# Kernel optimization log

Measured on AMD Instinct MI355X. Metric: run time of the kernel, lower is better.

## Reference

```python
import jax, jax.numpy as jnp
import numpy as np

IN, H, L = 512, 1024, 2
N, T = 64, 256


def setup_inputs() -> dict:
    key = jax.random.key(0)
    ks = jax.random.split(key, 1 + 4 * L)
    x = jax.random.normal(ks[0], (N, T, IN), dtype=jnp.float32)
    inp = {"x": x}
    for l in range(L):
        d_in = IN if l == 0 else H
        s_x = 1.0 / np.sqrt(d_in)
        s_h = 1.0 / np.sqrt(H)
        # concatenated gate order: [i, f, g, o]
        inp[f"Wx{l}"] = jax.random.normal(ks[1 + 4 * l], (4 * H, d_in), dtype=jnp.float32) * s_x
        inp[f"Wh{l}"] = jax.random.normal(ks[2 + 4 * l], (4 * H, H), dtype=jnp.float32) * s_h
        inp[f"b{l}"] = jax.random.normal(ks[3 + 4 * l], (4 * H,), dtype=jnp.float32) * 0.1
        # peephole weights for [i, f, o] (original inits these to zero; randomized here)
        inp[f"Wc{l}"] = jax.random.normal(ks[4 + 4 * l], (3, H), dtype=jnp.float32) * 0.1
    return inp


def _lstm_forward(x, params):
    # params: list of (Wx [4H,d_in], Wh [4H,H], b [4H], Wc [3,H]) per layer
    n = x.shape[0]
    h0 = jnp.zeros((L, n, H), dtype=x.dtype)
    c0 = jnp.zeros((L, n, H), dtype=x.dtype)

    def step(carry, x_t):
        hs, cs = carry
        new_h, new_c = [], []
        inp_t = x_t
        for l, (Wx, Wh, b, Wc) in enumerate(params):
            h, c = hs[l], cs[l]
            gates = inp_t @ Wx.T + h @ Wh.T + b  # [n, 4H]
            gi, gf, gg, go = jnp.split(gates, 4, axis=-1)
            i = jax.nn.sigmoid(gi + Wc[0] * c)
            f = jax.nn.sigmoid(gf + Wc[1] * c)  # computed but unused (faithful to source)
            g = jnp.tanh(gg)
            o = jax.nn.sigmoid(go + Wc[2] * c)
            ct = g * c + i * g          # faithful: forget gate not applied
            ht = o * jnp.tanh(c)        # faithful: uses OLD cell state
            new_h.append(ht)
            new_c.append(ct)
            inp_t = ht  # dropout p=0 -> identity
        hs = jnp.stack(new_h)
        cs = jnp.stack(new_c)
        return (hs, cs), new_h[-1]

    (hs, cs), outs = jax.lax.scan(step, (h0, c0), jnp.swapaxes(x, 0, 1))
    out = jnp.swapaxes(outs, 0, 1)  # [N, T, H]
    return out, (hs[-1], cs[-1])


def reference(x, Wx0, Wh0, b0, Wc0, Wx1, Wh1, b1, Wc1):
    params = [(Wx0, Wh0, b0, Wc0), (Wx1, Wh1, b1, Wc1)]
    return _lstm_forward(x, params)
```

## Files before the change

kernel.cpp:

```cpp
#include <hip/hip_runtime.h>
#include <stdint.h>


#define T_STEPS 256
#define HDIM    1024
#define NB      64
#define INDIM   512
#define NWG     256
#define TPB     256
#define PRING   8

typedef _Float16 f16;
typedef __attribute__((ext_vector_type(8))) _Float16 f16x8;
typedef __attribute__((ext_vector_type(4))) float    f32x4;

#define CNT_OFF 0
#define XB_OFF  81920
#define H0_OFF  16859136
#define H1_OFF  50544640
#define C0_OFF  84230144
#define C1_OFF  84492288
#define P0_OFF  84754432
#define P1_OFF  91045888

__device__ __forceinline__ float sigm(float x)     { return 1.0f / (1.0f + __expf(-x)); }
__device__ __forceinline__ float tanhfast(float x) { float e = __expf(2.0f * x); return 1.0f - 2.0f / (e + 1.0f); }

__device__ __forceinline__ void arrive(int* c) {
  __hip_atomic_fetch_add(c, 1, __ATOMIC_RELAXED, __HIP_MEMORY_SCOPE_AGENT);
}
__device__ __forceinline__ void wait_ge(int* c, int v) {
  while (__hip_atomic_load(c, __ATOMIC_RELAXED, __HIP_MEMORY_SCOPE_AGENT) < v)
    __builtin_amdgcn_s_sleep(1);
  __atomic_signal_fence(__ATOMIC_ACQUIRE);
}
__device__ __forceinline__ void sti(int* p, int v) {
  __hip_atomic_store(p, v, __ATOMIC_RELAXED, __HIP_MEMORY_SCOPE_AGENT);
}
__device__ __forceinline__ void st2h(f16* p, float a, float b) {
  union { f16 h[2]; uint32_t u; } cc; cc.h[0] = (f16)a; cc.h[1] = (f16)b;
  __hip_atomic_store((uint32_t*)p, cc.u, __ATOMIC_RELAXED, __HIP_MEMORY_SCOPE_AGENT);
}
__device__ __forceinline__ void st8a(void* p, unsigned long long v) {
  __hip_atomic_store((unsigned long long*)p, v, __ATOMIC_RELAXED, __HIP_MEMORY_SCOPE_AGENT);
}
__device__ __forceinline__ unsigned long long ld8(const float* p) {
  return __hip_atomic_load((const unsigned long long*)p, __ATOMIC_RELAXED, __HIP_MEMORY_SCOPE_AGENT);
}
__device__ __forceinline__ f16x8 pack8(f32x4 a, f32x4 b) {
  f16x8 h;
  h[0]=(f16)a[0]; h[1]=(f16)a[1]; h[2]=(f16)a[2]; h[3]=(f16)a[3];
  h[4]=(f16)b[0]; h[5]=(f16)b[1]; h[6]=(f16)b[2]; h[7]=(f16)b[3];
  return h;
}

template<int K>
__device__ __forceinline__ void gemm48_regB(const f16* __restrict__ Aw,
                                            const f16x8 (&B)[3][8],
                                            int lr, f32x4 (&acc)[4][3]) {
  constexpr int NIT = K / 128;
  const f16* a0 = Aw + (size_t)(lr +  0) * K;
  const f16* a1 = Aw + (size_t)(lr + 16) * K;
  const f16* a2 = Aw + (size_t)(lr + 32) * K;
  const f16* a3 = Aw + (size_t)(lr + 48) * K;
  f16x8 A0[NIT], A1[NIT], A2[NIT], A3[NIT];
#pragma unroll
  for (int it = 0; it < NIT; ++it) {
    const int kk = it * 32;
    A0[it] = *(const f16x8*)(a0 + kk);
    A1[it] = *(const f16x8*)(a1 + kk);
    A2[it] = *(const f16x8*)(a2 + kk);
    A3[it] = *(const f16x8*)(a3 + kk);
  }
#pragma unroll
  for (int it = 0; it < NIT; ++it) {
    acc[0][0] = __builtin_amdgcn_mfma_f32_16x16x32_f16(A0[it], B[0][it], acc[0][0], 0, 0, 0);
    acc[0][1] = __builtin_amdgcn_mfma_f32_16x16x32_f16(A0[it], B[1][it], acc[0][1], 0, 0, 0);
    acc[0][2] = __builtin_amdgcn_mfma_f32_16x16x32_f16(A0[it], B[2][it], acc[0][2], 0, 0, 0);
    acc[1][0] = __builtin_amdgcn_mfma_f32_16x16x32_f16(A1[it], B[0][it], acc[1][0], 0, 0, 0);
    acc[1][1] = __builtin_amdgcn_mfma_f32_16x16x32_f16(A1[it], B[1][it], acc[1][1], 0, 0, 0);
    acc[1][2] = __builtin_amdgcn_mfma_f32_16x16x32_f16(A1[it], B[2][it], acc[1][2], 0, 0, 0);
    acc[2][0] = __builtin_amdgcn_mfma_f32_16x16x32_f16(A2[it], B[0][it], acc[2][0], 0, 0, 0);
    acc[2][1] = __builtin_amdgcn_mfma_f32_16x16x32_f16(A2[it], B[1][it], acc[2][1], 0, 0, 0);
    acc[2][2] = __builtin_amdgcn_mfma_f32_16x16x32_f16(A2[it], B[2][it], acc[2][2], 0, 0, 0);
    acc[3][0] = __builtin_amdgcn_mfma_f32_16x16x32_f16(A3[it], B[0][it], acc[3][0], 0, 0, 0);
    acc[3][1] = __builtin_amdgcn_mfma_f32_16x16x32_f16(A3[it], B[1][it], acc[3][1], 0, 0, 0);
    acc[3][2] = __builtin_amdgcn_mfma_f32_16x16x32_f16(A3[it], B[2][it], acc[3][2], 0, 0, 0);
  }
}

__global__ __launch_bounds__(TPB, 1) void lstm_pers(
    const float* __restrict__ x,
    const float* __restrict__ Wx0, const float* __restrict__ Wh0,
    const float* __restrict__ b0,  const float* __restrict__ Wc0,
    const float* __restrict__ Wx1, const float* __restrict__ Wh1,
    const float* __restrict__ b1,  const float* __restrict__ Wc1,
    float* __restrict__ out, char* __restrict__ ws)
{
  int* cbase = (int*)(ws + CNT_OFF);
  int* proCnt = cbase;
  auto FLG = [&](int g, int i) { return cbase + 16 + ((g * 64 + i) << 4); };

  f16* XB   = (f16*)(ws + XB_OFF);
  f16* H0   = (f16*)(ws + H0_OFF);
  f16* H1   = (f16*)(ws + H1_OFF);
  float* C0 = (float*)(ws + C0_OFF);
  float* C1 = (float*)(ws + C1_OFF);
  float* P0b = (float*)(ws + P0_OFF);
  float* P1b = (float*)(ws + P1_OFF);

  __shared__ float lds[4][64][52];

  const int tid  = threadIdx.x;
  const int wg   = blockIdx.x;
  const int gtid = wg * TPB + tid;
  const int GSZ  = NWG * TPB;

  const int grp  = wg >> 6;
  const int ug   = wg & 63;
  const int lane = tid & 63;
  const int wv   = tid >> 6;
  const int quad = lane >> 4;
  const int lr   = lane & 15;

  const float* Wsrc; int K;
  switch (grp) {
    case 0:  Wsrc = Wx0; K = 512;  break;
    case 1:  Wsrc = Wh0; K = 1024; break;
    case 2:  Wsrc = Wx1; K = 1024; break;
    default: Wsrc = Wh1; K = 1024; break;
  }
  const int Kq  = K >> 2;
  const int NIT = K >> 7;

  f16x8 Breg[3][8];
#pragma unroll
  for (int nt = 0; nt < 3; ++nt) {
    const int R = ug * 16 + lr + (nt == 1 ? 2048 : (nt == 2 ? 3072 : 0));
    const float* wr = Wsrc + (size_t)R * K + wv * Kq + quad * 8;
#pragma unroll
    for (int it = 0; it < 8; ++it) {
      if (it < NIT) {
        f32x4 f0 = *(const f32x4*)(wr + it * 32);
        f32x4 f1 = *(const f32x4*)(wr + it * 32 + 4);
        Breg[nt][it] = pack8(f0, f1);
      } else {
        Breg[nt][it] = (f16x8){};
      }
    }
  }
  for (int idx = gtid; idx < T_STEPS * NB * 256; idx += GSZ) {
    int t = idx >> 14, n = (idx >> 8) & 63, i2 = (idx & 255) << 1;
    const float* src = x + (size_t)n * (T_STEPS * INDIM) + (size_t)t * INDIM + i2;
    st2h(&XB[(size_t)idx << 1], src[0], src[1]);
  }

  __builtin_amdgcn_s_waitcnt(0);
  __syncthreads();
  if (tid == 0) { arrive(proCnt); wait_ge(proCnt, NWG); }
  __syncthreads();

  float* cst = (grp == 1) ? C0 : C1;
  const int m_e = tid >> 2, j0 = (tid & 3) << 2;
  const int u0  = ug * 16 + j0;
  float* crow = cst + (size_t)m_e * HDIM + u0;

  f32x4 b_i{}, b_g{}, b_o{}, wci{}, wco{};
  if (grp & 1) {
    const float* bb = (grp == 1) ? b0 : b1;
    const float* wc = (grp == 1) ? Wc0 : Wc1;
    b_i = *(const f32x4*)(bb + u0);
    b_g = *(const f32x4*)(bb + 2048 + u0);
    b_o = *(const f32x4*)(bb + 3072 + u0);
    wci = *(const f32x4*)(wc + u0);
    wco = *(const f32x4*)(wc + 2048 + u0);
  }

  for (int t = 0; t < T_STEPS; ++t) {
    {
      int* myp = nullptr; int tgt = 0;
      if (grp == 0) {
        if (lane == 0 && t >= PRING) { myp = FLG(1, ug); tgt = t - PRING + 1; }
      } else if (grp == 1) {
        if (lane < 16 && t > 0)      { myp = FLG(1, wv * 16 + lr); tgt = t; }
        else if (lane == 16)         { myp = FLG(0, ug); tgt = t + 1; }
      } else if (grp == 2) {
        if (lane < 16)               { myp = FLG(1, wv * 16 + lr); tgt = t + 1; }
        else if (lane == 16 && t >= PRING) { myp = FLG(3, ug); tgt = t - PRING + 1; }
      } else {
        if (lane < 16 && t > 0)      { myp = FLG(3, wv * 16 + lr); tgt = t; }
        else if (lane == 16)         { myp = FLG(2, ug); tgt = t + 1; }
      }
      if (myp) {
        while (__hip_atomic_load(myp, __ATOMIC_RELAXED, __HIP_MEMORY_SCOPE_AGENT) < tgt)
          __builtin_amdgcn_s_sleep(1);
      }
      __atomic_signal_fence(__ATOMIC_ACQUIRE);
    }

    const f16* Abase;
    if (grp == 0)      Abase = XB + (size_t)t * NB * INDIM;
    else if (grp == 1) Abase = H0 + (size_t)t * NB * HDIM;
    else if (grp == 2) Abase = H0 + (size_t)(t + 1) * NB * HDIM;
    else               Abase = H1 + (size_t)t * NB * HDIM;

    unsigned long long pr0, pr1, pr2, pr3, pr4, pr5;
    f32x4 c4{};
    if (grp & 1) {
      const float* Pb = (grp == 1 ? P0b : P1b) + (size_t)(t & (PRING - 1)) * NB * 3072;
      const float* pbase = Pb + (size_t)m_e * 3072 + ug * 48 + j0;
      pr0 = ld8(pbase);      pr1 = ld8(pbase + 2);
      pr2 = ld8(pbase + 16); pr3 = ld8(pbase + 18);
      pr4 = ld8(pbase + 32); pr5 = ld8(pbase + 34);
      c4 = *(const f32x4*)crow;
    }

    f32x4 acc[4][3];
#pragma unroll
    for (int mt = 0; mt < 4; ++mt)
#pragma unroll
      for (int nt = 0; nt < 3; ++nt)
        acc[mt][nt] = (f32x4){0.f, 0.f, 0.f, 0.f};

    const f16* Aw = Abase + wv * Kq + quad * 8;
    if (grp == 0) gemm48_regB<512>(Aw, Breg, lr, acc);
    else          gemm48_regB<1024>(Aw, Breg, lr, acc);

#pragma unroll
    for (int mt = 0; mt < 4; ++mt)
#pragma unroll
      for (int nt = 0; nt < 3; ++nt)
#pragma unroll
        for (int r = 0; r < 4; ++r)
          lds[wv][mt * 16 + quad * 4 + r][nt * 16 + lr] = acc[mt][nt][r];
    __syncthreads();

    f32x4 hv, cn;
    if ((grp & 1) == 0) {
      float* Pb = (grp == 0 ? P0b : P1b) + (size_t)(t & (PRING - 1)) * NB * 3072;
#pragma unroll
      for (int r = 0; r < 6; ++r) {
        const int s  = r * 256 + tid;
        const int m  = s / 24, cp = s - m * 24;
        const int c0 = cp << 1;
        float v0 = lds[0][m][c0]     + lds[1][m][c0]     + lds[2][m][c0]     + lds[3][m][c0];
        float v1 = lds[0][m][c0 + 1] + lds[1][m][c0 + 1] + lds[2][m][c0 + 1] + lds[3][m][c0 + 1];
        union { float f[2]; unsigned long long u; } pp; pp.f[0] = v0; pp.f[1] = v1;
        st8a(Pb + (size_t)m * 3072 + ug * 48 + c0, pp.u);
      }
    } else {
      union { unsigned long long u; float f[2]; } q0, q1, q2, q3, q4, q5;
      q0.u = pr0; q1.u = pr1; q2.u = pr2; q3.u = pr3; q4.u = pr4; q5.u = pr5;
      f32x4 vi = (f32x4){0.f, 0.f, 0.f, 0.f};
      f32x4 vg = vi, vo = vi;
#pragma unroll
      for (int w = 0; w < 4; ++w) {
        vi += *(const f32x4*)&lds[w][m_e][j0];
        vg += *(const f32x4*)&lds[w][m_e][16 + j0];
        vo += *(const f32x4*)&lds[w][m_e][32 + j0];
      }
      const float pif[4] = {q0.f[0], q0.f[1], q1.f[0], q1.f[1]};
      const float pgf[4] = {q2.f[0], q2.f[1], q3.f[0], q3.f[1]};
      const float pof[4] = {q4.f[0], q4.f[1], q5.f[0], q5.f[1]};
      f16* Hdst = (grp == 1 ? H0 : H1) + (size_t)(t + 1) * NB * HDIM;
#pragma unroll
      for (int k = 0; k < 4; ++k) {
        float gi = vi[k] + pif[k] + b_i[k];
        float gg = vg[k] + pgf[k] + b_g[k];
        float go = vo[k] + pof[k] + b_o[k];
        float cold = c4[k];
        float iv = sigm(gi + wci[k] * cold);
        float gv = tanhfast(gg);
        float ov = sigm(go + wco[k] * cold);
        cn[k] = gv * (cold + iv);
        hv[k] = ov * tanhfast(cold);
      }
      *(f32x4*)crow = cn;
      union { f16 h[4]; unsigned long long u; } hh;
      hh.h[0]=(f16)hv[0]; hh.h[1]=(f16)hv[1]; hh.h[2]=(f16)hv[2]; hh.h[3]=(f16)hv[3];
      st8a(&Hdst[(size_t)m_e * HDIM + u0], hh.u);
    }

    __builtin_amdgcn_s_waitcnt(0);
    __syncthreads();
    if (tid == 0) sti(FLG(grp, ug), t + 1);

    if (grp == 3) {
      *(f32x4*)&out[(size_t)m_e * (T_STEPS * HDIM) + (size_t)t * HDIM + u0] = hv;
      if (t == T_STEPS - 1) {
        *(f32x4*)&out[(size_t)NB * T_STEPS * HDIM + (size_t)m_e * HDIM + u0] = hv;
        *(f32x4*)&out[(size_t)NB * T_STEPS * HDIM + NB * HDIM + (size_t)m_e * HDIM + u0] = cn;
      }
    }
  }
}

extern "C" void kernel_launch(void* const* d_in, const int* in_sizes, int n_in,
                              void* d_out, int out_size, void* d_ws, size_t ws_size,
                              hipStream_t stream) {
  const float* x   = (const float*)d_in[0];
  const float* Wx0 = (const float*)d_in[1];
  const float* Wh0 = (const float*)d_in[2];
  const float* b0  = (const float*)d_in[3];
  const float* Wc0 = (const float*)d_in[4];
  const float* Wx1 = (const float*)d_in[5];
  const float* Wh1 = (const float*)d_in[6];
  const float* b1  = (const float*)d_in[7];
  const float* Wc1 = (const float*)d_in[8];
  char* ws = (char*)d_ws;

  hipMemsetAsync(ws + CNT_OFF, 0, 81920, stream);
  hipMemsetAsync(ws + H0_OFF, 0, NB * HDIM * 2, stream);
  hipMemsetAsync(ws + H1_OFF, 0, NB * HDIM * 2, stream);
  hipMemsetAsync(ws + C0_OFF, 0, 2 * NB * HDIM * 4, stream);

  hipLaunchKernelGGL(lstm_pers, dim3(NWG), dim3(TPB), 0, stream,
                     x, Wx0, Wh0, b0, Wc0, Wx1, Wh1, b1, Wc1,
                     (float*)d_out, ws);
}
```

Measured before the change: 2.159 ms.

## Halve persistent workgroups, give each twice the hidden units

```diff
diff --git a/kernel.cpp b/kernel.cpp
--- a/kernel.cpp
+++ b/kernel.cpp
@@ -6,7 +6,7 @@
 #define HDIM    1024
 #define NB      64
 #define INDIM   512
-#define NWG     256
+#define NWG     128
 #define TPB     256
 #define PRING   8
 
@@ -53,39 +53,35 @@
   h[4]=(f16)b[0]; h[5]=(f16)b[1]; h[6]=(f16)b[2]; h[7]=(f16)b[3];
   return h;
 }
+__device__ __forceinline__ unsigned long long packh4(float a, float b, float c, float d) {
+  union { f16 h[4]; unsigned long long u; } hh;
+  hh.h[0]=(f16)a; hh.h[1]=(f16)b; hh.h[2]=(f16)c; hh.h[3]=(f16)d;
+  return hh.u;
+}
 
 template<int K>
-__device__ __forceinline__ void gemm48_regB(const f16* __restrict__ Aw,
-                                            const f16x8 (&B)[3][8],
-                                            int lr, f32x4 (&acc)[4][3]) {
+__device__ __forceinline__ void gemm96(const f16* __restrict__ Aw,
+                                       const f16x8 (&B)[6][8],
+                                       int lr, f32x4 (&acc)[4][6]) {
   constexpr int NIT = K / 128;
   const f16* a0 = Aw + (size_t)(lr +  0) * K;
   const f16* a1 = Aw + (size_t)(lr + 16) * K;
   const f16* a2 = Aw + (size_t)(lr + 32) * K;
   const f16* a3 = Aw + (size_t)(lr + 48) * K;
-  f16x8 A0[NIT], A1[NIT], A2[NIT], A3[NIT];
 #pragma unroll
   for (int it = 0; it < NIT; ++it) {
     const int kk = it * 32;
-    A0[it] = *(const f16x8*)(a0 + kk);
-    A1[it] = *(const f16x8*)(a1 + kk);
-    A2[it] = *(const f16x8*)(a2 + kk);
-    A3[it] = *(const f16x8*)(a3 + kk);
-  }
-#pragma unroll
-  for (int it = 0; it < NIT; ++it) {
-    acc[0][0] = __builtin_amdgcn_mfma_f32_16x16x32_f16(A0[it], B[0][it], acc[0][0], 0, 0, 0);
-    acc[0][1] = __builtin_amdgcn_mfma_f32_16x16x32_f16(A0[it], B[1][it], acc[0][1], 0, 0, 0);
-    acc[0][2] = __builtin_amdgcn_mfma_f32_16x16x32_f16(A0[it], B[2][it], acc[0][2], 0, 0, 0);
-    acc[1][0] = __builtin_amdgcn_mfma_f32_16x16x32_f16(A1[it], B[0][it], acc[1][0], 0, 0, 0);
-    acc[1][1] = __builtin_amdgcn_mfma_f32_16x16x32_f16(A1[it], B[1][it], acc[1][1], 0, 0, 0);
-    acc[1][2] = __builtin_amdgcn_mfma_f32_16x16x32_f16(A1[it], B[2][it], acc[1][2], 0, 0, 0);
-    acc[2][0] = __builtin_amdgcn_mfma_f32_16x16x32_f16(A2[it], B[0][it], acc[2][0], 0, 0, 0);
-    acc[2][1] = __builtin_amdgcn_mfma_f32_16x16x32_f16(A2[it], B[1][it], acc[2][1], 0, 0, 0);
-    acc[2][2] = __builtin_amdgcn_mfma_f32_16x16x32_f16(A2[it], B[2][it], acc[2][2], 0, 0, 0);
-    acc[3][0] = __builtin_amdgcn_mfma_f32_16x16x32_f16(A3[it], B[0][it], acc[3][0], 0, 0, 0);
-    acc[3][1] = __builtin_amdgcn_mfma_f32_16x16x32_f16(A3[it], B[1][it], acc[3][1], 0, 0, 0);
-    acc[3][2] = __builtin_amdgcn_mfma_f32_16x16x32_f16(A3[it], B[2][it], acc[3][2], 0, 0, 0);
+    f16x8 A0 = *(const f16x8*)(a0 + kk);
+    f16x8 A1 = *(const f16x8*)(a1 + kk);
+    f16x8 A2 = *(const f16x8*)(a2 + kk);
+    f16x8 A3 = *(const f16x8*)(a3 + kk);
+#pragma unroll
+    for (int nt = 0; nt < 6; ++nt) {
+      acc[0][nt] = __builtin_amdgcn_mfma_f32_16x16x32_f16(A0, B[nt][it], acc[0][nt], 0, 0, 0);
+      acc[1][nt] = __builtin_amdgcn_mfma_f32_16x16x32_f16(A1, B[nt][it], acc[1][nt], 0, 0, 0);
+      acc[2][nt] = __builtin_amdgcn_mfma_f32_16x16x32_f16(A2, B[nt][it], acc[2][nt], 0, 0, 0);
+      acc[3][nt] = __builtin_amdgcn_mfma_f32_16x16x32_f16(A3, B[nt][it], acc[3][nt], 0, 0, 0);
+    }
   }
 }
 
@@ -99,7 +95,7 @@
 {
   int* cbase = (int*)(ws + CNT_OFF);
   int* proCnt = cbase;
-  auto FLG = [&](int g, int i) { return cbase + 16 + ((g * 64 + i) << 4); };
+  auto FLG = [&](int g, int i) { return cbase + 16 + ((g * 32 + i) << 4); };
 
   f16* XB   = (f16*)(ws + XB_OFF);
   f16* H0   = (f16*)(ws + H0_OFF);
@@ -109,15 +105,15 @@
   float* P0b = (float*)(ws + P0_OFF);
   float* P1b = (float*)(ws + P1_OFF);
 
-  __shared__ float lds[4][64][52];
+  __shared__ float lds[4][64][100];
 
   const int tid  = threadIdx.x;
   const int wg   = blockIdx.x;
   const int gtid = wg * TPB + tid;
   const int GSZ  = NWG * TPB;
 
-  const int grp  = wg >> 6;
-  const int ug   = wg & 63;
+  const int grp  = wg >> 5;
+  const int ug   = wg & 31;
   const int lane = tid & 63;
   const int wv   = tid >> 6;
   const int quad = lane >> 4;
@@ -133,10 +129,12 @@
   const int Kq  = K >> 2;
   const int NIT = K >> 7;
 
-  f16x8 Breg[3][8];
-#pragma unroll
-  for (int nt = 0; nt < 3; ++nt) {
-    const int R = ug * 16 + lr + (nt == 1 ? 2048 : (nt == 2 ? 3072 : 0));
+  f16x8 Breg[6][8];
+#pragma unroll
+  for (int nt = 0; nt < 6; ++nt) {
+    const int gate = nt >> 1;
+    const int R = ug * 32 + (nt & 1) * 16 + lr
+                + (gate == 1 ? 2048 : (gate == 2 ? 3072 : 0));
     const float* wr = Wsrc + (size_t)R * K + wv * Kq + quad * 8;
 #pragma unroll
     for (int it = 0; it < 8; ++it) {
@@ -161,20 +159,11 @@
   __syncthreads();
 
   float* cst = (grp == 1) ? C0 : C1;
-  const int m_e = tid >> 2, j0 = (tid & 3) << 2;
-  const int u0  = ug * 16 + j0;
+  const int m_e = tid >> 2, j0 = (tid & 3) << 3;
+  const int u0  = ug * 32 + j0;
   float* crow = cst + (size_t)m_e * HDIM + u0;
-
-  f32x4 b_i{}, b_g{}, b_o{}, wci{}, wco{};
-  if (grp & 1) {
-    const float* bb = (grp == 1) ? b0 : b1;
-    const float* wc = (grp == 1) ? Wc0 : Wc1;
-    b_i = *(const f32x4*)(bb + u0);
-    b_g = *(const f32x4*)(bb + 2048 + u0);
-    b_o = *(const f32x4*)(bb + 3072 + u0);
-    wci = *(const f32x4*)(wc + u0);
-    wco = *(const f32x4*)(wc + 2048 + u0);
-  }
+  const float* bb = (grp == 1) ? b0 : b1;
+  const float* wc = (grp == 1) ? Wc0 : Wc1;
 
   for (int t = 0; t < T_STEPS; ++t) {
     {
@@ -182,14 +171,14 @@
       if (grp == 0) {
         if (lane == 0 && t >= PRING) { myp = FLG(1, ug); tgt = t - PRING + 1; }
       } else if (grp == 1) {
-        if (lane < 16 && t > 0)      { myp = FLG(1, wv * 16 + lr); tgt = t; }
-        else if (lane == 16)         { myp = FLG(0, ug); tgt = t + 1; }
+        if (lane < 8 && t > 0)       { myp = FLG(1, wv * 8 + lane); tgt = t; }
+        else if (lane == 8)          { myp = FLG(0, ug); tgt = t + 1; }
       } else if (grp == 2) {
-        if (lane < 16)               { myp = FLG(1, wv * 16 + lr); tgt = t + 1; }
-        else if (lane == 16 && t >= PRING) { myp = FLG(3, ug); tgt = t - PRING + 1; }
+        if (lane < 8)                { myp = FLG(1, wv * 8 + lane); tgt = t + 1; }
+        else if (lane == 8 && t >= PRING) { myp = FLG(3, ug); tgt = t - PRING + 1; }
       } else {
-        if (lane < 16 && t > 0)      { myp = FLG(3, wv * 16 + lr); tgt = t; }
-        else if (lane == 16)         { myp = FLG(2, ug); tgt = t + 1; }
+        if (lane < 8 && t > 0)       { myp = FLG(3, wv * 8 + lane); tgt = t; }
+        else if (lane == 8)          { myp = FLG(2, ug); tgt = t + 1; }
       }
       if (myp) {
         while (__hip_atomic_load(myp, __ATOMIC_RELAXED, __HIP_MEMORY_SCOPE_AGENT) < tgt)
@@ -204,81 +193,103 @@
     else if (grp == 2) Abase = H0 + (size_t)(t + 1) * NB * HDIM;
     else               Abase = H1 + (size_t)t * NB * HDIM;
 
-    unsigned long long pr0, pr1, pr2, pr3, pr4, pr5;
-    f32x4 c4{};
+    unsigned long long pri[4], prg[4], pro[4];
+    f32x4 c4[2], bi[2], bg[2], bo[2], wi[2], wo[2];
     if (grp & 1) {
       const float* Pb = (grp == 1 ? P0b : P1b) + (size_t)(t & (PRING - 1)) * NB * 3072;
-      const float* pbase = Pb + (size_t)m_e * 3072 + ug * 48 + j0;
-      pr0 = ld8(pbase);      pr1 = ld8(pbase + 2);
-      pr2 = ld8(pbase + 16); pr3 = ld8(pbase + 18);
-      pr4 = ld8(pbase + 32); pr5 = ld8(pbase + 34);
-      c4 = *(const f32x4*)crow;
-    }
-
-    f32x4 acc[4][3];
+      const float* pbase = Pb + (size_t)m_e * 3072 + ug * 96 + j0;
+#pragma unroll
+      for (int q = 0; q < 4; ++q) {
+        pri[q] = ld8(pbase + 2 * q);
+        prg[q] = ld8(pbase + 32 + 2 * q);
+        pro[q] = ld8(pbase + 64 + 2 * q);
+      }
+#pragma unroll
+      for (int p = 0; p < 2; ++p) {
+        c4[p] = *(const f32x4*)(crow + 4 * p);
+        bi[p] = *(const f32x4*)(bb + u0 + 4 * p);
+        bg[p] = *(const f32x4*)(bb + 2048 + u0 + 4 * p);
+        bo[p] = *(const f32x4*)(bb + 3072 + u0 + 4 * p);
+        wi[p] = *(const f32x4*)(wc + u0 + 4 * p);
+        wo[p] = *(const f32x4*)(wc + 2048 + u0 + 4 * p);
+      }
+    }
+
+    f32x4 acc[4][6];
 #pragma unroll
     for (int mt = 0; mt < 4; ++mt)
 #pragma unroll
-      for (int nt = 0; nt < 3; ++nt)
+      for (int nt = 0; nt < 6; ++nt)
         acc[mt][nt] = (f32x4){0.f, 0.f, 0.f, 0.f};
 
     const f16* Aw = Abase + wv * Kq + quad * 8;
-    if (grp == 0) gemm48_regB<512>(Aw, Breg, lr, acc);
-    else          gemm48_regB<1024>(Aw, Breg, lr, acc);
+    if (grp == 0) gemm96<512>(Aw, Breg, lr, acc);
+    else          gemm96<1024>(Aw, Breg, lr, acc);
 
 #pragma unroll
     for (int mt = 0; mt < 4; ++mt)
 #pragma unroll
-      for (int nt = 0; nt < 3; ++nt)
+      for (int nt = 0; nt < 6; ++nt)
 #pragma unroll
         for (int r = 0; r < 4; ++r)
           lds[wv][mt * 16 + quad * 4 + r][nt * 16 + lr] = acc[mt][nt][r];
     __syncthreads();
 
-    f32x4 hv, cn;
+    f32x4 hv[2], cn[2];
     if ((grp & 1) == 0) {
       float* Pb = (grp == 0 ? P0b : P1b) + (size_t)(t & (PRING - 1)) * NB * 3072;
 #pragma unroll
-      for (int r = 0; r < 6; ++r) {
+      for (int r = 0; r < 12; ++r) {
         const int s  = r * 256 + tid;
-        const int m  = s / 24, cp = s - m * 24;
+        const int m  = s / 48, cp = s - m * 48;
         const int c0 = cp << 1;
         float v0 = lds[0][m][c0]     + lds[1][m][c0]     + lds[2][m][c0]     + lds[3][m][c0];
         float v1 = lds[0][m][c0 + 1] + lds[1][m][c0 + 1] + lds[2][m][c0 + 1] + lds[3][m][c0 + 1];
         union { float f[2]; unsigned long long u; } pp; pp.f[0] = v0; pp.f[1] = v1;
-        st8a(Pb + (size_t)m * 3072 + ug * 48 + c0, pp.u);
+        st8a(Pb + (size_t)m * 3072 + ug * 96 + c0, pp.u);
       }
     } else {
-      union { unsigned long long u; float f[2]; } q0, q1, q2, q3, q4, q5;
-      q0.u = pr0; q1.u = pr1; q2.u = pr2; q3.u = pr3; q4.u = pr4; q5.u = pr5;
-      f32x4 vi = (f32x4){0.f, 0.f, 0.f, 0.f};
-      f32x4 vg = vi, vo = vi;
-#pragma unroll
-      for (int w = 0; w < 4; ++w) {
-        vi += *(const f32x4*)&lds[w][m_e][j0];
-        vg += *(const f32x4*)&lds[w][m_e][16 + j0];
-        vo += *(const f32x4*)&lds[w][m_e][32 + j0];
-      }
-      const float pif[4] = {q0.f[0], q0.f[1], q1.f[0], q1.f[1]};
-      const float pgf[4] = {q2.f[0], q2.f[1], q3.f[0], q3.f[1]};
-      const float pof[4] = {q4.f[0], q4.f[1], q5.f[0], q5.f[1]};
+      f32x4 vi[2], vg[2], vo[2];
+#pragma unroll
+      for (int p = 0; p < 2; ++p) { vi[p] = (f32x4){0,0,0,0}; vg[p] = vi[p]; vo[p] = vi[p]; }
+#pragma unroll
+      for (int w = 0; w < 4; ++w)
+#pragma unroll
+        for (int p = 0; p < 2; ++p) {
+          vi[p] += *(const f32x4*)&lds[w][m_e][j0 + 4 * p];
+          vg[p] += *(const f32x4*)&lds[w][m_e][32 + j0 + 4 * p];
+          vo[p] += *(const f32x4*)&lds[w][m_e][64 + j0 + 4 * p];
+        }
+      float pif[8], pgf[8], pof[8];
+      union { unsigned long long u; float f[2]; } qq;
+#pragma unroll
+      for (int q = 0; q < 4; ++q) {
+        qq.u = pri[q]; pif[2*q] = qq.f[0]; pif[2*q+1] = qq.f[1];
+        qq.u = prg[q]; pgf[2*q] = qq.f[0]; pgf[2*q+1] = qq.f[1];
+        qq.u = pro[q]; pof[2*q] = qq.f[0]; pof[2*q+1] = qq.f[1];
+      }
       f16* Hdst = (grp == 1 ? H0 : H1) + (size_t)(t + 1) * NB * HDIM;
 #pragma unroll
-      for (int k = 0; k < 4; ++k) {
-        float gi = vi[k] + pif[k] + b_i[k];
-        float gg = vg[k] + pgf[k] + b_g[k];
-        float go = vo[k] + pof[k] + b_o[k];
-        float cold = c4[k];
-        float iv = sigm(gi + wci[k] * cold);
-        float gv = tanhfast(gg);
-        float ov = sigm(go + wco[k] * cold);
-        cn[k] = gv * (cold + iv);
-        hv[k] = ov * tanhfast(cold);
-      }
-      *(f32x4*)crow = cn;
-      union { f16 h[4]; unsigned long long u; } hh;
-      hh.h[0]=(f16)hv[0]; hh.h[1]=(f16)hv[1]; hh.h[2]=(f16)hv[2]; hh.h[3]=(f16)hv[3];
-      st8a(&Hdst[(size_t)m_e * HDIM + u0], hh.u);
+      for (int p = 0; p < 2; ++p)
+#pragma unroll
+        for (int k = 0; k < 4; ++k) {
+          const int e = 4 * p + k;
+          float gi = vi[p][k] + pif[e] + bi[p][k];
+          float gg = vg[p][k] + pgf[e] + bg[p][k];
+          float go = vo[p][k] + pof[e] + bo[p][k];
+          float cold = c4[p][k];
+          float iv = sigm(gi + wi[p][k] * cold);
+          float gv = tanhfast(gg);
+          float ov = sigm(go + wo[p][k] * cold);
+          cn[p][k] = gv * (cold + iv);
+          hv[p][k] = ov * tanhfast(cold);
+        }
+#pragma unroll
+      for (int p = 0; p < 2; ++p) {
+        *(f32x4*)(crow + 4 * p) = cn[p];
+        st8a(&Hdst[(size_t)m_e * HDIM + u0 + 4 * p],
+             packh4(hv[p][0], hv[p][1], hv[p][2], hv[p][3]));
+      }
     }
 
     __builtin_amdgcn_s_waitcnt(0);
@@ -286,10 +297,14 @@
     if (tid == 0) sti(FLG(grp, ug), t + 1);
 
     if (grp == 3) {
-      *(f32x4*)&out[(size_t)m_e * (T_STEPS * HDIM) + (size_t)t * HDIM + u0] = hv;
+      float* ob = &out[(size_t)m_e * (T_STEPS * HDIM) + (size_t)t * HDIM + u0];
+      *(f32x4*)ob = hv[0];
+      *(f32x4*)(ob + 4) = hv[1];
       if (t == T_STEPS - 1) {
-        *(f32x4*)&out[(size_t)NB * T_STEPS * HDIM + (size_t)m_e * HDIM + u0] = hv;
-        *(f32x4*)&out[(size_t)NB * T_STEPS * HDIM + NB * HDIM + (size_t)m_e * HDIM + u0] = cn;
+        float* hf = &out[(size_t)NB * T_STEPS * HDIM + (size_t)m_e * HDIM + u0];
+        float* cf = hf + (size_t)NB * HDIM;
+        *(f32x4*)hf = hv[0]; *(f32x4*)(hf + 4) = hv[1];
+        *(f32x4*)cf = cn[0]; *(f32x4*)(cf + 4) = cn[1];
       }
     }
   }
```

New measurement: 3.105 ms. 1.44x slower.
